# Kernel tuning notes

Measured on AMD Instinct MI355X. Metric: run time of the kernel, lower is better.

Reference implementation:

```python
import jax, jax.numpy as jnp
import numpy as np

W_SEG = 2048   # segment length w
R = 4          # dilation rate
OFFSET = 0     # offset < r
H = 16         # num heads
C = 1024       # embed dim
M = W_SEG // R # tokens attended per segment


def _mha(xi, w_in, b_in, w_out, b_out):
    # xi: (b, s, m, c) -> causal multi-head self-attention per segment
    b, s, m, c = xi.shape
    dh = c // H
    qkv = jnp.einsum('bsmc,ec->bsme', xi, w_in) + b_in  # e = 3c
    q, k, v = jnp.split(qkv, 3, axis=-1)
    q = q.reshape(b, s, m, H, dh)
    k = k.reshape(b, s, m, H, dh)
    v = v.reshape(b, s, m, H, dh)
    scores = jnp.einsum('bsqhd,bskhd->bshqk', q, k) / jnp.sqrt(jnp.asarray(dh, xi.dtype))
    causal = jnp.tril(jnp.ones((m, m), dtype=bool))
    scores = jnp.where(causal, scores, jnp.asarray(-1e9, xi.dtype))
    p = jax.nn.softmax(scores, axis=-1)
    o = jnp.einsum('bshqk,bskhd->bsqhd', p, v).reshape(b, s, m, c)
    return jnp.einsum('bsmc,oc->bsmo', o, w_out) + b_out


def setup_inputs() -> dict:
    key = jax.random.key(0)
    k1, k2, k3, k4, k5 = jax.random.split(key, 5)
    x = jax.random.normal(k1, (4, 8192, C), dtype=jnp.float32)
    w_in = jax.random.normal(k2, (3 * C, C), dtype=jnp.float32) * (C ** -0.5)
    b_in = jnp.zeros((3 * C,), dtype=jnp.float32)
    w_out = jax.random.normal(k3, (C, C), dtype=jnp.float32) * (C ** -0.5)
    b_out = jnp.zeros((C,), dtype=jnp.float32)
    return {"x": x, "w_in": w_in, "b_in": b_in, "w_out": w_out, "b_out": b_out}


def reference(x, w_in, b_in, w_out, b_out):
    b, n, c = x.shape
    s = n // W_SEG  # number of segments
    xr = x.reshape(b, s, W_SEG, c)
    xi = xr[:, :, OFFSET::R, :]                # (b, s, m, c) dilated gather
    oi = _mha(xi, w_in, b_in, w_out, b_out)    # attention per segment
    out = jnp.zeros_like(xr).at[:, :, OFFSET::R, :].set(oi)  # scatter (disjoint indices)
    return out.reshape(b, n, c)
```

## Files before the change

### kernel.cpp

```cpp
#include <hip/hip_runtime.h>


typedef unsigned short u16;
typedef short short8 __attribute__((ext_vector_type(8)));
typedef short short4v __attribute__((ext_vector_type(4)));
typedef float f32x4 __attribute__((ext_vector_type(4)));

__device__ __forceinline__ u16 f2bf(float f) {
  unsigned u = __builtin_bit_cast(unsigned, f);
  u += 0x7FFFu + ((u >> 16) & 1u);
  return (u16)(u >> 16);
}

__device__ __forceinline__ void gload_lds16(const void* g, void* l) {
  __builtin_amdgcn_global_load_lds((const __attribute__((address_space(1))) void*)g,
                                   (__attribute__((address_space(3))) void*)l,
                                   16, 0, 0);
}

#define SBAR() asm volatile("s_barrier" ::: "memory")

__global__ void conv_gather(const float* __restrict__ x, u16* __restrict__ xi) {
  int t = blockIdx.x * 256 + threadIdx.x;
  if (t >= (8192 * 1024) / 8) return;
  int row = t >> 7;
  int col = (t & 127) << 3;
  size_t src = ((size_t)((row >> 9) << 11) + ((row & 511) << 2)) * 1024 + col;
  float4 v0 = *(const float4*)(x + src);
  float4 v1 = *(const float4*)(x + src + 4);
  short8 o;
  o[0] = f2bf(v0.x); o[1] = f2bf(v0.y); o[2] = f2bf(v0.z); o[3] = f2bf(v0.w);
  o[4] = f2bf(v1.x); o[5] = f2bf(v1.y); o[6] = f2bf(v1.z); o[7] = f2bf(v1.w);
  *(short8*)(xi + (size_t)row * 1024 + col) = o;
}

__global__ void conv_plain(const float* __restrict__ in, u16* __restrict__ out, int n8) {
  int t = blockIdx.x * 256 + threadIdx.x;
  if (t >= n8) return;
  size_t base = (size_t)t * 8;
  float4 v0 = *(const float4*)(in + base);
  float4 v1 = *(const float4*)(in + base + 4);
  short8 o;
  o[0] = f2bf(v0.x); o[1] = f2bf(v0.y); o[2] = f2bf(v0.z); o[3] = f2bf(v0.w);
  o[4] = f2bf(v1.x); o[5] = f2bf(v1.y); o[6] = f2bf(v1.z); o[7] = f2bf(v1.w);
  *(short8*)(out + base) = o;
}

__global__ __launch_bounds__(512) void gemm_qkv8(
    const u16* __restrict__ A, const u16* __restrict__ B,
    const float* __restrict__ bias, u16* __restrict__ C) {
  constexpr int K = 1024, NT = 16;
  __shared__ u16 lds[3][24576];

  const int tid = threadIdx.x;
  const int w = tid >> 6, lane = tid & 63;
  const int wm = w >> 2, wn = w & 3;
  const int g = lane >> 4, lq = lane & 15;

  const int s = (blockIdx.x & 7) * 96 + (blockIdx.x >> 3);
  const int m0 = (s / 12) * 128, n0 = (s % 12) * 256;

  const int srow = w * 8 + (lane >> 3);
  const int jch = (lane & 7) ^ ((lane >> 3) & 7);
  const u16* Ab = A + (size_t)(m0 + srow) * K + jch * 8;
  const u16* Bb = B + (size_t)(n0 + srow) * K + jch * 8;
  const int ldst = w * 512 + lane * 8;

#define SA(buf_, qd, kt) gload_lds16(Ab + (size_t)(qd) * 64 * K + (kt) * 64, &lds[buf_][(qd) * 4096 + ldst])
#define SB(buf_, qd, kt) gload_lds16(Bb + (size_t)(qd) * 64 * K + (kt) * 64, &lds[buf_][8192 + (qd) * 4096 + ldst])

  const int xw = lq & 7;
  const int arow = wm * 64 + lq;
  const int brow = wn * 64 + lq;

#define RDA(kc)                                                                   \
  _Pragma("unroll") for (int mi = 0; mi < 4; ++mi)                                \
      af[mi] = *(const short8*)(&lds[buf][(arow + mi * 16) * 64 + (((kc) * 4 + g) ^ xw) * 8]);
#define RDB(kc)                                                                   \
  _Pragma("unroll") for (int ni = 0; ni < 4; ++ni)                                \
      bf[ni] = *(const short8*)(&lds[buf][8192 + (brow + ni * 16) * 64 + (((kc) * 4 + g) ^ xw) * 8]);
#define MFMA16()                                                                  \
  __builtin_amdgcn_s_setprio(1);                                                  \
  _Pragma("unroll") for (int mi = 0; mi < 4; ++mi)                                \
      _Pragma("unroll") for (int ni = 0; ni < 4; ++ni)                            \
          acc[mi][ni] = __builtin_amdgcn_mfma_f32_16x16x32_bf16(                  \
              af[mi], bf[ni], acc[mi][ni], 0, 0, 0);                              \
  __builtin_amdgcn_s_setprio(0);

  f32x4 acc[4][4] = {};

  SA(0, 0, 0); SA(0, 1, 0); SB(0, 0, 0); SB(0, 1, 0); SB(0, 2, 0); SB(0, 3, 0);
  SA(1, 0, 1); SA(1, 1, 1); SB(1, 0, 1); SB(1, 1, 1); SB(1, 2, 1); SB(1, 3, 1);
  asm volatile("s_waitcnt vmcnt(6)" ::: "memory");
  SBAR();

#pragma unroll 1
  for (int t = 0; t < NT; ++t) {
    const int buf = t % 3, nb = (t + 2) % 3;
    short8 af[4], bf[4];

    if (t + 2 < NT) { SA(nb, 0, t + 2); SA(nb, 1, t + 2); SB(nb, 0, t + 2); }
    RDA(0); RDB(0);
    SBAR();
    MFMA16();
    SBAR();

    if (t + 2 < NT) { SB(nb, 1, t + 2); SB(nb, 2, t + 2); SB(nb, 3, t + 2); }
    RDA(1); RDB(1);
    if (t + 2 < NT) { asm volatile("s_waitcnt vmcnt(6)" ::: "memory"); }
    else            { asm volatile("s_waitcnt vmcnt(0)" ::: "memory"); }
    SBAR();
    MFMA16();
    SBAR();
  }

  if (n0 < 2048) {
#pragma unroll
    for (int mi = 0; mi < 4; ++mi) {
#pragma unroll
      for (int ni = 0; ni < 4; ++ni) {
        const int col = n0 + wn * 64 + ni * 16 + lq;
        const float bv = bias[col];
        u16* dst = C + (size_t)(col >> 10) * 8388608 + (col & 1023);
#pragma unroll
        for (int r = 0; r < 4; ++r) {
          const int m = m0 + wm * 64 + mi * 16 + g * 4 + r;
          dst[(size_t)m * 1024] = f2bf(acc[mi][ni][r] + bv);
        }
      }
    }
  } else {
    u16* vt = C + 16777216;
#pragma unroll
    for (int mi = 0; mi < 4; ++mi) {
      const int m4 = m0 + wm * 64 + mi * 16 + g * 4;
      const int bs = m4 >> 9, k = m4 & 511;
#pragma unroll
      for (int ni = 0; ni < 4; ++ni) {
        const int cv = n0 - 2048 + wn * 64 + ni * 16 + lq;
        const int h = cv >> 6, d = cv & 63;
        const float bv = bias[cv + 2048];
        short4v pk;
#pragma unroll
        for (int r = 0; r < 4; ++r) pk[r] = (short)f2bf(acc[mi][ni][r] + bv);
        *(short4v*)(&vt[(size_t)((bs * 16 + h) * 64 + d) * 512 + k]) = pk;
      }
    }
  }
#undef SA
#undef SB
#undef RDA
#undef RDB
#undef MFMA16
}

__global__ __launch_bounds__(256) void gemm_out(
    const u16* __restrict__ A, const u16* __restrict__ B,
    const float* __restrict__ bias, float* __restrict__ Cout,
    int M, int N, int K) {
  __shared__ u16 As[128 * 32];
  __shared__ u16 Bs[128 * 32];
  const int tid = threadIdx.x;
  const int w = tid >> 6, lane = tid & 63;
  const int wr = w >> 1, wc = w & 1;
  const int g = lane >> 4, lq = lane & 15;
  const int m0 = blockIdx.x * 128, n0 = blockIdx.y * 128;
  const int sr = w * 16 + (lane >> 2);
  const int sc = (lane & 3) * 8;
  f32x4 acc[4][4] = {};

  for (int k0 = 0; k0 < K; k0 += 32) {
    gload_lds16(A + (size_t)(m0 + sr) * K + k0 + sc,      &As[sr * 32 + sc]);
    gload_lds16(A + (size_t)(m0 + 64 + sr) * K + k0 + sc, &As[(64 + sr) * 32 + sc]);
    gload_lds16(B + (size_t)(n0 + sr) * K + k0 + sc,      &Bs[sr * 32 + sc]);
    gload_lds16(B + (size_t)(n0 + 64 + sr) * K + k0 + sc, &Bs[(64 + sr) * 32 + sc]);
    __syncthreads();

    short8 af[4], bf[4];
#pragma unroll
    for (int i = 0; i < 4; ++i) {
      af[i] = *reinterpret_cast<const short8*>(&As[(wr * 64 + i * 16 + lq) * 32 + g * 8]);
      bf[i] = *reinterpret_cast<const short8*>(&Bs[(wc * 64 + i * 16 + lq) * 32 + g * 8]);
    }
#pragma unroll
    for (int mi = 0; mi < 4; ++mi)
#pragma unroll
      for (int ni = 0; ni < 4; ++ni)
        acc[mi][ni] = __builtin_amdgcn_mfma_f32_16x16x32_bf16(af[mi], bf[ni], acc[mi][ni], 0, 0, 0);
    __syncthreads();
  }

#pragma unroll
  for (int mi = 0; mi < 4; ++mi) {
#pragma unroll
    for (int ni = 0; ni < 4; ++ni) {
      const int col = n0 + wc * 64 + ni * 16 + lq;
      const float bv = bias[col];
#pragma unroll
      for (int r = 0; r < 4; ++r) {
        const int m = m0 + wr * 64 + mi * 16 + g * 4 + r;
        const int orow = ((m >> 9) << 11) + ((m & 511) << 2);
        Cout[(size_t)orow * 1024 + col] = acc[mi][ni][r] + bv;
      }
    }
  }

  for (int i = 0; i < 48; ++i) {
    const int idx = i * 256 + tid;
    const int z = idx >> 12;
    const int mm = (idx & 4095) >> 5;
    const int ch = idx & 31;
    const int m = m0 + mm;
    const int orow = ((m >> 9) << 11) + ((m & 511) << 2) + 1 + z;
    *(float4*)(Cout + (size_t)orow * 1024 + n0 + ch * 4) =
        make_float4(0.f, 0.f, 0.f, 0.f);
  }
}

__global__ __launch_bounds__(512) void attn_kernel(const u16* __restrict__ qkv,
                                                   u16* __restrict__ o_ws) {
  __shared__ u16 Ks[512 * 64];
  __shared__ u16 Vs[64 * 512];
  __shared__ u16 Pl[8][16][40];

  const int tid = threadIdx.x;
  const int w = tid >> 6, lane = tid & 63;
  const int g = lane >> 4, lq = lane & 15;
  const int bh = blockIdx.x;
  const int bs = bh >> 4, h = bh & 15;

  const u16* baseq = qkv + (size_t)bs * 512 * 1024 + h * 64;
  const u16* basek = qkv + 8388608 + (size_t)bs * 512 * 1024 + h * 64;
  const u16* vhead = qkv + 16777216 + (size_t)bh * 32768;

  {
    const int rsub = lane >> 3;
    const int csw = (lane & 7) ^ rsub;
#pragma unroll
    for (int i = 0; i < 8; ++i) {
      const int step = i * 8 + w;
      gload_lds16(basek + (size_t)(step * 8 + rsub) * 1024 + csw * 8,
                  &Ks[step * 512 + lane * 8]);
    }
#pragma unroll
    for (int i = 0; i < 8; ++i) {
      const int d = i * 8 + w;
      gload_lds16(vhead + (size_t)d * 512 + (lane ^ (d & 7)) * 8,
                  &Vs[d * 512 + lane * 8]);
    }
  }
  __syncthreads();

  const int xw = lq & 7;
#pragma unroll 1
  for (int qi = 0; qi < 4; ++qi) {
    const int qt = ((qi & 1) ? (15 - w) : w) + (qi >> 1) * 16;
    const int q0 = qt * 16;
    const short8 qf0 = *(const short8*)(baseq + (size_t)(q0 + lq) * 1024 + g * 8);
    const short8 qf1 = *(const short8*)(baseq + (size_t)(q0 + lq) * 1024 + 32 + g * 8);
    f32x4 oacc[4] = {};
    float l_r[4] = {0.f, 0.f, 0.f, 0.f};
    const int nst = (qt + 2) >> 1;
#pragma unroll 1
    for (int kk = 0; kk < nst; ++kk) {
      const int kb = kk * 32;
      const bool last = (kk == nst - 1);
      f32x4 s[2];
#pragma unroll
      for (int tt = 0; tt < 2; ++tt) {
        const int r = kb + tt * 16 + lq;
        short8 klo = *(const short8*)(&Ks[r * 64 + ((g ^ xw) * 8)]);
        short8 khi = *(const short8*)(&Ks[r * 64 + (((4 + g) ^ xw) * 8)]);
        f32x4 z = {};
        z = __builtin_amdgcn_mfma_f32_16x16x32_bf16(qf0, klo, z, 0, 0, 0);
        z = __builtin_amdgcn_mfma_f32_16x16x32_bf16(qf1, khi, z, 0, 0, 0);
        s[tt] = z;
      }
#pragma unroll
      for (int tt = 0; tt < 2; ++tt) {
#pragma unroll
        for (int r = 0; r < 4; ++r) {
          float p = __expf(s[tt][r] * 0.125f);
          if (last && (kb + tt * 16 + lq > q0 + g * 4 + r)) p = 0.f;
          l_r[r] += p;
          Pl[w][g * 4 + r][tt * 16 + lq] = f2bf(p);
        }
      }
      short8 pf = *(const short8*)(&Pl[w][lq][g * 8]);
#pragma unroll
      for (int dt = 0; dt < 4; ++dt) {
        const int vr = dt * 16 + lq;
        short8 vf = *(const short8*)(&Vs[vr * 512 + ((((kb >> 3) + g) ^ xw) * 8)]);
        oacc[dt] = __builtin_amdgcn_mfma_f32_16x16x32_bf16(pf, vf, oacc[dt], 0, 0, 0);
      }
    }
#pragma unroll
    for (int r = 0; r < 4; ++r) {
      float l = l_r[r];
      l += __shfl_xor(l, 1);
      l += __shfl_xor(l, 2);
      l += __shfl_xor(l, 4);
      l += __shfl_xor(l, 8);
      const float inv = 1.0f / l;
      const int q = q0 + g * 4 + r;
      u16* dst = o_ws + (size_t)(bs * 512 + q) * 1024 + h * 64;
#pragma unroll
      for (int dt = 0; dt < 4; ++dt) dst[dt * 16 + lq] = f2bf(oacc[dt][r] * inv);
    }
  }
}

extern "C" void kernel_launch(void* const* d_in, const int* in_sizes, int n_in,
                              void* d_out, int out_size, void* d_ws, size_t ws_size,
                              hipStream_t stream) {
  const float* x     = (const float*)d_in[0];
  const float* w_in  = (const float*)d_in[1];
  const float* b_in  = (const float*)d_in[2];
  const float* w_out = (const float*)d_in[3];
  const float* b_out = (const float*)d_in[4];

  char* ws = (char*)d_ws;
  u16* xi_bf   = (u16*)(ws);
  u16* win_bf  = (u16*)(ws + 16777216);
  u16* wout_bf = (u16*)(ws + 16777216 + 6291456);
  u16* qkv     = (u16*)(ws + 16777216 + 6291456 + 2097152);
  u16* o_bf    = (u16*)(ws + 16777216 + 6291456 + 2097152 + 50331648);

  conv_gather<<<4096, 256, 0, stream>>>(x, xi_bf);
  conv_plain<<<1536, 256, 0, stream>>>(w_in, win_bf, (3072 * 1024) / 8);
  conv_plain<<<512, 256, 0, stream>>>(w_out, wout_bf, (1024 * 1024) / 8);
  gemm_qkv8<<<768, 512, 0, stream>>>(xi_bf, win_bf, b_in, qkv);
  attn_kernel<<<256, 512, 0, stream>>>(qkv, o_bf);
  gemm_out<<<dim3(64, 8), 256, 0, stream>>>(o_bf, wout_bf, b_out, (float*)d_out, 8192, 1024, 1024);
}
```

Before: 155.4 us.

## Reuse pipelined triple-buffer GEMM for output projection and restructure k-loop schedule

Turns the QKV GEMM into a template that also handles the output projection, replacing the simple single-buffered gemm_out with the 3-stage direct-to-LDS pipelined kernel using 128x256 tiles. The main loop now issues all six next-stage loads at once, reads both k-chunks of fragments up front, and runs 32 MFMAs between one pair of barriers instead of two half-steps. The intent is fewer barriers and better latency hiding for both GEMMs. The trade-off is more registers for fragments, and the output GEMM now launches only 256 blocks, which may leave compute units underused.

Result: faster. 147.8 us (-4.9%).

```diff
diff --git a/kernel.cpp b/kernel.cpp
--- a/kernel.cpp
+++ b/kernel.cpp
@@ -46,10 +46,11 @@
   *(short8*)(out + base) = o;
 }
 
-__global__ __launch_bounds__(512) void gemm_qkv8(
+template <int NCOLS, int MODE>
+__global__ __launch_bounds__(512) void gemm_pipe(
     const u16* __restrict__ A, const u16* __restrict__ B,
-    const float* __restrict__ bias, u16* __restrict__ C) {
-  constexpr int K = 1024, NT = 16;
+    const float* __restrict__ bias, void* __restrict__ Cout) {
+  constexpr int K = 1024, NT = 16, NTILE = NCOLS / 256;
   __shared__ u16 lds[3][24576];
 
   const int tid = threadIdx.x;
@@ -57,8 +58,9 @@
   const int wm = w >> 2, wn = w & 3;
   const int g = lane >> 4, lq = lane & 15;
 
-  const int s = (blockIdx.x & 7) * 96 + (blockIdx.x >> 3);
-  const int m0 = (s / 12) * 128, n0 = (s % 12) * 256;
+  const int per = gridDim.x >> 3;
+  const int s = (blockIdx.x & 7) * per + (blockIdx.x >> 3);
+  const int m0 = (s / NTILE) * 128, n0 = (s % NTILE) * 256;
 
   const int srow = w * 8 + (lane >> 3);
   const int jch = (lane & 7) ^ ((lane >> 3) & 7);
@@ -73,19 +75,12 @@
   const int arow = wm * 64 + lq;
   const int brow = wn * 64 + lq;
 
-#define RDA(kc)                                                                   \
+#define RDA(dst_, kc)                                                             \
   _Pragma("unroll") for (int mi = 0; mi < 4; ++mi)                                \
-      af[mi] = *(const short8*)(&lds[buf][(arow + mi * 16) * 64 + (((kc) * 4 + g) ^ xw) * 8]);
-#define RDB(kc)                                                                   \
+      dst_[mi] = *(const short8*)(&lds[buf][(arow + mi * 16) * 64 + (((kc) * 4 + g) ^ xw) * 8]);
+#define RDB(dst_, kc)                                                             \
   _Pragma("unroll") for (int ni = 0; ni < 4; ++ni)                                \
-      bf[ni] = *(const short8*)(&lds[buf][8192 + (brow + ni * 16) * 64 + (((kc) * 4 + g) ^ xw) * 8]);
-#define MFMA16()                                                                  \
-  __builtin_amdgcn_s_setprio(1);                                                  \
-  _Pragma("unroll") for (int mi = 0; mi < 4; ++mi)                                \
-      _Pragma("unroll") for (int ni = 0; ni < 4; ++ni)                            \
-          acc[mi][ni] = __builtin_amdgcn_mfma_f32_16x16x32_bf16(                  \
-              af[mi], bf[ni], acc[mi][ni], 0, 0, 0);                              \
-  __builtin_amdgcn_s_setprio(0);
+      dst_[ni] = *(const short8*)(&lds[buf][8192 + (brow + ni * 16) * 64 + (((kc) * 4 + g) ^ xw) * 8]);
 
   f32x4 acc[4][4] = {};
 
@@ -97,124 +92,97 @@
 #pragma unroll 1
   for (int t = 0; t < NT; ++t) {
     const int buf = t % 3, nb = (t + 2) % 3;
-    short8 af[4], bf[4];
-
-    if (t + 2 < NT) { SA(nb, 0, t + 2); SA(nb, 1, t + 2); SB(nb, 0, t + 2); }
-    RDA(0); RDB(0);
-    SBAR();
-    MFMA16();
-    SBAR();
-
-    if (t + 2 < NT) { SB(nb, 1, t + 2); SB(nb, 2, t + 2); SB(nb, 3, t + 2); }
-    RDA(1); RDB(1);
+    short8 a0[4], b0[4], a1[4], b1[4];
+
+    if (t + 2 < NT) {
+      SA(nb, 0, t + 2); SA(nb, 1, t + 2);
+      SB(nb, 0, t + 2); SB(nb, 1, t + 2); SB(nb, 2, t + 2); SB(nb, 3, t + 2);
+    }
+    RDA(a0, 0); RDB(b0, 0); RDA(a1, 1); RDB(b1, 1);
     if (t + 2 < NT) { asm volatile("s_waitcnt vmcnt(6)" ::: "memory"); }
     else            { asm volatile("s_waitcnt vmcnt(0)" ::: "memory"); }
     SBAR();
-    MFMA16();
+    __builtin_amdgcn_s_setprio(1);
+#pragma unroll
+    for (int mi = 0; mi < 4; ++mi)
+#pragma unroll
+      for (int ni = 0; ni < 4; ++ni)
+        acc[mi][ni] = __builtin_amdgcn_mfma_f32_16x16x32_bf16(a0[mi], b0[ni], acc[mi][ni], 0, 0, 0);
+#pragma unroll
+    for (int mi = 0; mi < 4; ++mi)
+#pragma unroll
+      for (int ni = 0; ni < 4; ++ni)
+        acc[mi][ni] = __builtin_amdgcn_mfma_f32_16x16x32_bf16(a1[mi], b1[ni], acc[mi][ni], 0, 0, 0);
+    __builtin_amdgcn_s_setprio(0);
     SBAR();
   }
 
-  if (n0 < 2048) {
+  if (MODE == 0) {
+    u16* C = (u16*)Cout;
+    if (n0 < 2048) {
+#pragma unroll
+      for (int mi = 0; mi < 4; ++mi) {
+#pragma unroll
+        for (int ni = 0; ni < 4; ++ni) {
+          const int col = n0 + wn * 64 + ni * 16 + lq;
+          const float bv = bias[col];
+          u16* dst = C + (size_t)(col >> 10) * 8388608 + (col & 1023);
+#pragma unroll
+          for (int r = 0; r < 4; ++r) {
+            const int m = m0 + wm * 64 + mi * 16 + g * 4 + r;
+            dst[(size_t)m * 1024] = f2bf(acc[mi][ni][r] + bv);
+          }
+        }
+      }
+    } else {
+      u16* vt = C + 16777216;
+#pragma unroll
+      for (int mi = 0; mi < 4; ++mi) {
+        const int m4 = m0 + wm * 64 + mi * 16 + g * 4;
+        const int bs = m4 >> 9, k = m4 & 511;
+#pragma unroll
+        for (int ni = 0; ni < 4; ++ni) {
+          const int cv = n0 - 2048 + wn * 64 + ni * 16 + lq;
+          const int h = cv >> 6, d = cv & 63;
+          const float bv = bias[cv + 2048];
+          short4v pk;
+#pragma unroll
+          for (int r = 0; r < 4; ++r) pk[r] = (short)f2bf(acc[mi][ni][r] + bv);
+          *(short4v*)(&vt[(size_t)((bs * 16 + h) * 64 + d) * 512 + k]) = pk;
+        }
+      }
+    }
+  } else {
+    float* O = (float*)Cout;
 #pragma unroll
     for (int mi = 0; mi < 4; ++mi) {
 #pragma unroll
       for (int ni = 0; ni < 4; ++ni) {
         const int col = n0 + wn * 64 + ni * 16 + lq;
         const float bv = bias[col];
-        u16* dst = C + (size_t)(col >> 10) * 8388608 + (col & 1023);
 #pragma unroll
         for (int r = 0; r < 4; ++r) {
           const int m = m0 + wm * 64 + mi * 16 + g * 4 + r;
-          dst[(size_t)m * 1024] = f2bf(acc[mi][ni][r] + bv);
+          const int orow = ((m >> 9) << 11) + ((m & 511) << 2);
+          O[(size_t)orow * 1024 + col] = acc[mi][ni][r] + bv;
         }
       }
     }
-  } else {
-    u16* vt = C + 16777216;
-#pragma unroll
-    for (int mi = 0; mi < 4; ++mi) {
-      const int m4 = m0 + wm * 64 + mi * 16 + g * 4;
-      const int bs = m4 >> 9, k = m4 & 511;
-#pragma unroll
-      for (int ni = 0; ni < 4; ++ni) {
-        const int cv = n0 - 2048 + wn * 64 + ni * 16 + lq;
-        const int h = cv >> 6, d = cv & 63;
-        const float bv = bias[cv + 2048];
-        short4v pk;
-#pragma unroll
-        for (int r = 0; r < 4; ++r) pk[r] = (short)f2bf(acc[mi][ni][r] + bv);
-        *(short4v*)(&vt[(size_t)((bs * 16 + h) * 64 + d) * 512 + k]) = pk;
-      }
+    for (int i = 0; i < 48; ++i) {
+      const int idx = i * 512 + tid;
+      const int z = idx >> 13;
+      const int mm = (idx & 8191) >> 6;
+      const int ch = idx & 63;
+      const int m = m0 + mm;
+      const int orow = ((m >> 9) << 11) + ((m & 511) << 2) + 1 + z;
+      *(float4*)(O + (size_t)orow * 1024 + n0 + ch * 4) =
+          make_float4(0.f, 0.f, 0.f, 0.f);
     }
   }
 #undef SA
 #undef SB
 #undef RDA
 #undef RDB
-#undef MFMA16
-}
-
-__global__ __launch_bounds__(256) void gemm_out(
-    const u16* __restrict__ A, const u16* __restrict__ B,
-    const float* __restrict__ bias, float* __restrict__ Cout,
-    int M, int N, int K) {
-  __shared__ u16 As[128 * 32];
-  __shared__ u16 Bs[128 * 32];
-  const int tid = threadIdx.x;
-  const int w = tid >> 6, lane = tid & 63;
-  const int wr = w >> 1, wc = w & 1;
-  const int g = lane >> 4, lq = lane & 15;
-  const int m0 = blockIdx.x * 128, n0 = blockIdx.y * 128;
-  const int sr = w * 16 + (lane >> 2);
-  const int sc = (lane & 3) * 8;
-  f32x4 acc[4][4] = {};
-
-  for (int k0 = 0; k0 < K; k0 += 32) {
-    gload_lds16(A + (size_t)(m0 + sr) * K + k0 + sc,      &As[sr * 32 + sc]);
-    gload_lds16(A + (size_t)(m0 + 64 + sr) * K + k0 + sc, &As[(64 + sr) * 32 + sc]);
-    gload_lds16(B + (size_t)(n0 + sr) * K + k0 + sc,      &Bs[sr * 32 + sc]);
-    gload_lds16(B + (size_t)(n0 + 64 + sr) * K + k0 + sc, &Bs[(64 + sr) * 32 + sc]);
-    __syncthreads();
-
-    short8 af[4], bf[4];
-#pragma unroll
-    for (int i = 0; i < 4; ++i) {
-      af[i] = *reinterpret_cast<const short8*>(&As[(wr * 64 + i * 16 + lq) * 32 + g * 8]);
-      bf[i] = *reinterpret_cast<const short8*>(&Bs[(wc * 64 + i * 16 + lq) * 32 + g * 8]);
-    }
-#pragma unroll
-    for (int mi = 0; mi < 4; ++mi)
-#pragma unroll
-      for (int ni = 0; ni < 4; ++ni)
-        acc[mi][ni] = __builtin_amdgcn_mfma_f32_16x16x32_bf16(af[mi], bf[ni], acc[mi][ni], 0, 0, 0);
-    __syncthreads();
-  }
-
-#pragma unroll
-  for (int mi = 0; mi < 4; ++mi) {
-#pragma unroll
-    for (int ni = 0; ni < 4; ++ni) {
-      const int col = n0 + wc * 64 + ni * 16 + lq;
-      const float bv = bias[col];
-#pragma unroll
-      for (int r = 0; r < 4; ++r) {
-        const int m = m0 + wr * 64 + mi * 16 + g * 4 + r;
-        const int orow = ((m >> 9) << 11) + ((m & 511) << 2);
-        Cout[(size_t)orow * 1024 + col] = acc[mi][ni][r] + bv;
-      }
-    }
-  }
-
-  for (int i = 0; i < 48; ++i) {
-    const int idx = i * 256 + tid;
-    const int z = idx >> 12;
-    const int mm = (idx & 4095) >> 5;
-    const int ch = idx & 31;
-    const int m = m0 + mm;
-    const int orow = ((m >> 9) << 11) + ((m & 511) << 2) + 1 + z;
-    *(float4*)(Cout + (size_t)orow * 1024 + n0 + ch * 4) =
-        make_float4(0.f, 0.f, 0.f, 0.f);
-  }
 }
 
 __global__ __launch_bounds__(512) void attn_kernel(const u16* __restrict__ qkv,
@@ -329,7 +297,7 @@
   conv_gather<<<4096, 256, 0, stream>>>(x, xi_bf);
   conv_plain<<<1536, 256, 0, stream>>>(w_in, win_bf, (3072 * 1024) / 8);
   conv_plain<<<512, 256, 0, stream>>>(w_out, wout_bf, (1024 * 1024) / 8);
-  gemm_qkv8<<<768, 512, 0, stream>>>(xi_bf, win_bf, b_in, qkv);
+  gemm_pipe<3072, 0><<<768, 512, 0, stream>>>(xi_bf, win_bf, b_in, qkv);
   attn_kernel<<<256, 512, 0, stream>>>(qkv, o_bf);
-  gemm_out<<<dim3(64, 8), 256, 0, stream>>>(o_bf, wout_bf, b_out, (float*)d_out, 8192, 1024, 1024);
-}
+  gemm_pipe<1024, 1><<<256, 512, 0, stream>>>(o_bf, wout_bf, b_out, d_out);
+}
```
